# Kernel optimization log

Hardware: AMD Instinct MI355X
Metric: run time of the kernel (lower is better)

## Reference

```python
import jax, jax.numpy as jnp
import numpy as np
import itertools

# ---- constants matching init_kwargs ----
ED, KD, NH, AR = 512, 16, 8, 4
D = AR * KD            # 64 == ED // NH (required by cascade residual add)
DH = D * NH            # 512
RES, WS = 28, 7
SCALE = KD ** -0.5
KS = [7, 5, 3, 3, 3, 3, 3, 3]

# relative-position bias index map for a WSxWS window (49 unique |offset| pairs)
def _bias_idx(ws):
    pts = list(itertools.product(range(ws), range(ws)))
    offs, idxs = {}, []
    for p1 in pts:
        for p2 in pts:
            o = (abs(p1[0] - p2[0]), abs(p1[1] - p2[1]))
            if o not in offs:
                offs[o] = len(offs)
            idxs.append(offs[o])
    return np.array(idxs, dtype=np.int32).reshape(ws * ws, ws * ws), len(offs)
BIAS_IDX, N_OFFS = _bias_idx(WS)  # [49,49], 49


def dwconv(x, w, b):
    """Depthwise conv, stride 1, SAME padding (pad = k//2, odd k). w: [C,1,k,k]."""
    y = jax.lax.conv_general_dilated(x, w, (1, 1), 'SAME',
                                     dimension_numbers=('NCHW', 'OIHW', 'NCHW'),
                                     feature_group_count=x.shape[1])
    return y + b[None, :, None, None]


def pw(x, w, b):
    """1x1 conv (fused Conv2d_BN in eval mode). w: [O,C]."""
    return jnp.einsum('bchw,oc->bohw', x, w) + b[None, :, None, None]


def mlp(x, w1, b1, w2, b2):
    return pw(jax.nn.hard_swish(pw(x, w1, b1)), w2, b2)


def window_partition(x, ws):
    B, C, H, W = x.shape
    nH, nW = H // ws, W // ws
    return x.reshape(B, C, nH, ws, nW, ws).transpose(0, 2, 4, 1, 3, 5).reshape(B * nH * nW, C, ws, ws)


def window_merge(xw, B, H, W, ws):
    nH, nW = H // ws, W // ws
    C = xw.shape[1]
    return xw.reshape(B, nH, nW, C, ws, ws).transpose(0, 3, 1, 4, 2, 5).reshape(B, C, H, W)


def cascade_attention(xw, qkv_w, qkv_b, dwq_ws, dwq_bs, ab, proj_w, proj_b):
    """xw: [Bw, ED, WS, WS]; ab: [NH, N, N] bias table gathered per head."""
    Bw, C, H, W = xw.shape
    N = H * W
    spx = jnp.split(xw, NH, axis=1)          # NH chunks of [Bw, ED//NH, H, W]
    sp = spx[0]
    outs = []
    for i in range(NH):  # heads are structurally distinct (kernel sizes) -> Python loop ok
        if i > 0:
            sp = sp + spx[i]
        y = pw(sp, qkv_w[i], qkv_b[i])       # [Bw, 2*KD+D, H, W]
        q, k, v = jnp.split(y, [KD, 2 * KD], axis=1)
        q = dwconv(q, dwq_ws[i], dwq_bs[i])  # per-head depthwise conv on q
        qf = q.reshape(Bw, KD, N)
        kf = k.reshape(Bw, KD, N)
        vf = v.reshape(Bw, D, N)
        attn = jnp.einsum('bcn,bcm->bnm', qf, kf) * SCALE + ab[i]
        attn = jax.nn.softmax(attn, axis=-1)
        sp = jnp.einsum('bdm,bnm->bdn', vf, attn).reshape(Bw, D, H, W)
        outs.append(sp)
    y = jnp.concatenate(outs, axis=1)        # [Bw, DH, H, W]
    y = jax.nn.hard_swish(y)                 # proj = Sequential(act, Conv2d_BN)
    return pw(y, proj_w, proj_b)


def _forward(x, dw0_w, dw0_b, ffn0_w1, ffn0_b1, ffn0_w2, ffn0_b2,
             qkv_w, qkv_b, dwq_w7, dwq_b7, dwq_w5, dwq_b5, dwq_w3, dwq_b3,
             attn_bias, proj_w, proj_b,
             dw1_w, dw1_b, ffn1_w1, ffn1_b1, ffn1_w2, ffn1_b2):
    B, C, H, W = x.shape
    dwq_ws = [dwq_w7, dwq_w5] + [dwq_w3[i] for i in range(6)]
    dwq_bs = [dwq_b7, dwq_b5] + [dwq_b3[i] for i in range(6)]
    ab = attn_bias[:, BIAS_IDX]              # [NH, 49, 49]
    x = x + dwconv(x, dw0_w, dw0_b)
    x = x + mlp(x, ffn0_w1, ffn0_b1, ffn0_w2, ffn0_b2)
    xw = window_partition(x, WS)
    aw = cascade_attention(xw, qkv_w, qkv_b, dwq_ws, dwq_bs, ab, proj_w, proj_b)
    x = x + window_merge(aw, B, H, W, WS)
    x = x + dwconv(x, dw1_w, dw1_b)
    x = x + mlp(x, ffn1_w1, ffn1_b1, ffn1_w2, ffn1_b2)
    return x


def setup_inputs() -> dict:
    key = jax.random.key(0)
    ks = jax.random.split(key, 24)
    B = 64
    r = lambda k, shape, s=0.05: (jax.random.normal(k, shape, dtype=jnp.float32) * s)
    qkv_out = 2 * KD + D  # 96
    inp = {
        'x': jax.random.normal(ks[0], (B, ED, RES, RES), dtype=jnp.float32),
        'dw0_w': r(ks[1], (ED, 1, 3, 3)), 'dw0_b': r(ks[2], (ED,)),
        'ffn0_w1': r(ks[3], (2 * ED, ED)), 'ffn0_b1': r(ks[4], (2 * ED,)),
        'ffn0_w2': r(ks[5], (ED, 2 * ED)), 'ffn0_b2': r(ks[6], (ED,)),
        'qkv_w': r(ks[7], (NH, qkv_out, ED // NH)), 'qkv_b': r(ks[8], (NH, qkv_out)),
        'dwq_w7': r(ks[9], (KD, 1, 7, 7)), 'dwq_b7': r(ks[10], (KD,)),
        'dwq_w5': r(ks[11], (KD, 1, 5, 5)), 'dwq_b5': r(ks[12], (KD,)),
        'dwq_w3': r(ks[13], (6, KD, 1, 3, 3)), 'dwq_b3': r(ks[14], (6, KD)),
        'attn_bias': r(ks[15], (NH, N_OFFS)),
        'proj_w': r(ks[16], (ED, DH)), 'proj_b': r(ks[17], (ED,)),
        'dw1_w': r(ks[18], (ED, 1, 3, 3)), 'dw1_b': r(ks[19], (ED,)),
        'ffn1_w1': r(ks[20], (2 * ED, ED)), 'ffn1_b1': r(ks[21], (2 * ED,)),
        'ffn1_w2': r(ks[22], (ED, 2 * ED)), 'ffn1_b2': r(ks[23], (ED,)),
    }
    return inp


def reference(x, dw0_w, dw0_b, ffn0_w1, ffn0_b1, ffn0_w2, ffn0_b2,
              qkv_w, qkv_b, dwq_w7, dwq_b7, dwq_w5, dwq_b5, dwq_w3, dwq_b3,
              attn_bias, proj_w, proj_b,
              dw1_w, dw1_b, ffn1_w1, ffn1_b1, ffn1_w2, ffn1_b2):
    return _forward(x, dw0_w, dw0_b, ffn0_w1, ffn0_b1, ffn0_w2, ffn0_b2,
                    qkv_w, qkv_b, dwq_w7, dwq_b7, dwq_w5, dwq_b5, dwq_w3, dwq_b3,
                    attn_bias, proj_w, proj_b,
                    dw1_w, dw1_b, ffn1_w1, ffn1_b1, ffn1_w2, ffn1_b2)
```

## Files before the change

kernel.cpp:

```cpp
#include <hip/hip_runtime.h>
#include <hip/hip_bf16.h>


#define NPOS 50176
#define NEL ((size_t)512 * NPOS)

typedef __hip_bfloat16 hbf;
typedef __attribute__((ext_vector_type(8))) short short8;
typedef __attribute__((ext_vector_type(4))) short bf16x4;
typedef __attribute__((ext_vector_type(4))) float f32x4;

__device__ __forceinline__ float hswish(float v) {
    float t = fminf(fmaxf(v + 3.0f, 0.0f), 6.0f);
    return v * t * (1.0f / 6.0f);
}
__device__ __forceinline__ float b2f(hbf x) { return __bfloat162float(x); }
__device__ __forceinline__ hbf f2b(float x) { return __float2bfloat16(x); }

__device__ __forceinline__ unsigned short bfb(float v) {
    hbf h = f2b(v); unsigned short u; __builtin_memcpy(&u, &h, 2); return u;
}
__device__ __forceinline__ unsigned pk2(float a, float b) {
    return (unsigned)bfb(a) | ((unsigned)bfb(b) << 16);
}
__device__ __forceinline__ int swz128(int row, int b) {
    return row * 128 + (b ^ ((row & 7) << 4));
}

__device__ __forceinline__ bool is_bf16_buf(const void* probe) {
    const unsigned* w = (const unsigned*)probe;
    int hits = 0;
#pragma unroll
    for (int i = 0; i < 64; i++) {
        unsigned lo = w[i] & 0xFFFFu;
        unsigned e = (lo >> 7) & 0xFFu;
        hits += ((e >= 100u && e <= 140u) || lo == 0u) ? 1 : 0;
    }
    return hits >= 32;
}

#define OFF_W01  0
#define OFF_W02  524288
#define OFF_W11  1048576
#define OFF_W12  1572864
#define OFF_PW   2097152
#define OFF_QKVW 2359296
#define OFF_QKVB 2408448
#define OFF_W7   2409216
#define OFF_B7   2410000
#define OFF_W5   2410016
#define OFF_B5   2410416
#define OFF_W3   2410432
#define OFF_B3   2411296
#define OFF_AB   2411392
#define OFF_D0W  2411784
#define OFF_D0B  2416392
#define OFF_D1W  2416904
#define OFF_D1B  2421512
#define OFF_B01  2422024
#define OFF_B02  2423048
#define OFF_B11  2423560
#define OFF_B12  2424584
#define OFF_PB   2425096
#define ARENA_TOT 2425608

struct CvtArgs { const void* src; int off; int count; };
struct CvtTable { CvtArgs t[23]; };

__global__ __launch_bounds__(256) void k_convert(CvtTable tab, hbf* __restrict__ arena,
                                                 const void* __restrict__ probe) {
    CvtArgs a = tab.t[blockIdx.y];
    int i = blockIdx.x * 256 + threadIdx.x;
    if (i >= a.count) return;
    bool isbf = is_bf16_buf(probe);
    float v = isbf ? b2f(((const hbf*)a.src)[i]) : ((const float*)a.src)[i];
    arena[a.off + i] = f2b(v);
}

template <int EPI, int K>
__global__ __launch_bounds__(256) void k_gemm(const hbf* __restrict__ A,
                                              const hbf* __restrict__ B,
                                              const hbf* __restrict__ bias,
                                              const void* __restrict__ res,
                                              void* __restrict__ out,
                                              const void* __restrict__ probe) {
    __shared__ short sA[128 * 40];
    __shared__ short sB[128 * 40];

    const int tid = threadIdx.x;
    const int wave = tid >> 6, lane = tid & 63;
    const int col = lane & 15, quad = lane >> 4;
    const int m0 = blockIdx.x * 128, n0 = blockIdx.y * 128;
    const int wm = (wave & 1) * 64, wn = (wave >> 1) * 64;

    const int r0 = tid >> 2, c0 = tid & 3;
    const int r1 = 64 + (tid >> 2), c1 = tid & 3;

    f32x4 acc[4][4];
#pragma unroll
    for (int i = 0; i < 4; i++)
#pragma unroll
        for (int j = 0; j < 4; j++) acc[i][j] = (f32x4){0.f, 0.f, 0.f, 0.f};

    short8 pA0 = *(const short8*)(A + (size_t)(m0 + r0) * K + c0 * 8);
    short8 pA1 = *(const short8*)(A + (size_t)(m0 + r1) * K + c1 * 8);
    short8 pB0 = *(const short8*)(B + (size_t)(n0 + r0) * K + c0 * 8);
    short8 pB1 = *(const short8*)(B + (size_t)(n0 + r1) * K + c1 * 8);

    for (int k0 = 0; k0 < K; k0 += 32) {
        __syncthreads();
        *(short8*)(sA + r0 * 40 + c0 * 8) = pA0;
        *(short8*)(sA + r1 * 40 + c1 * 8) = pA1;
        *(short8*)(sB + r0 * 40 + c0 * 8) = pB0;
        *(short8*)(sB + r1 * 40 + c1 * 8) = pB1;
        if (k0 + 32 < K) {
            pA0 = *(const short8*)(A + (size_t)(m0 + r0) * K + k0 + 32 + c0 * 8);
            pA1 = *(const short8*)(A + (size_t)(m0 + r1) * K + k0 + 32 + c1 * 8);
            pB0 = *(const short8*)(B + (size_t)(n0 + r0) * K + k0 + 32 + c0 * 8);
            pB1 = *(const short8*)(B + (size_t)(n0 + r1) * K + k0 + 32 + c1 * 8);
        }
        __syncthreads();

        short8 af[4], bfr[4];
#pragma unroll
        for (int i = 0; i < 4; i++)
            af[i] = *(const short8*)(sA + (wm + i * 16 + col) * 40 + quad * 8);
#pragma unroll
        for (int j = 0; j < 4; j++)
            bfr[j] = *(const short8*)(sB + (wn + j * 16 + col) * 40 + quad * 8);
#pragma unroll
        for (int i = 0; i < 4; i++)
#pragma unroll
            for (int j = 0; j < 4; j++)
                acc[i][j] = __builtin_amdgcn_mfma_f32_16x16x32_bf16(af[i], bfr[j], acc[i][j], 0, 0, 0);
    }

    bool outbf = false;
    if constexpr (EPI == 3) outbf = is_bf16_buf(probe);

#pragma unroll
    for (int i = 0; i < 4; i++) {
#pragma unroll
        for (int j = 0; j < 4; j++) {
#pragma unroll
            for (int r = 0; r < 4; r++) {
                int mi = m0 + wm + i * 16 + quad * 4 + r;
                int nj = n0 + wn + j * 16 + col;
                float v = acc[i][j][r];
                if constexpr (EPI == 0) {
                    v = hswish(v + b2f(bias[nj]));
                    ((hbf*)out)[(size_t)mi * 1024 + nj] = f2b(v);
                } else if constexpr (EPI == 1) {
                    v += b2f(bias[mi]) + b2f(((const hbf*)res)[(size_t)nj * 512 + mi]);
                    ((float*)out)[(size_t)mi * NPOS + nj] = v;
                } else if constexpr (EPI == 2) {
                    int w = nj / 49, p = nj % 49;
                    int nct = (w >> 4) * 784 + (((w >> 2) & 3) * 7 + p / 7) * 28 + (w & 3) * 7 + p % 7;
                    size_t oi = (size_t)mi * NPOS + nct;
                    v += b2f(bias[mi]) + ((const float*)res)[oi];
                    ((float*)out)[oi] = v;
                } else {
                    int b = nj / 784, hw = nj % 784;
                    v += b2f(bias[mi]) + ((const float*)res)[(size_t)mi * NPOS + nj];
                    size_t oi = ((size_t)b * 512 + mi) * 784 + hw;
                    if (outbf) ((hbf*)out)[oi] = f2b(v);
                    else ((float*)out)[oi] = v;
                }
            }
        }
    }
}

template <int MODE, bool ISBF>
__device__ void dw_body(float* sIn, float* sW, const void* __restrict__ in,
                        const hbf* __restrict__ w, const hbf* __restrict__ bias,
                        hbf* __restrict__ outNK, float* __restrict__ outCT) {
    const int tid = threadIdx.x;
    const int tx = tid & 63, tg = tid >> 6;
    const int n0 = blockIdx.x * 64, c0 = blockIdx.y * 64;

    for (int e = tid; e < 640; e += 256) {
        int cc = e / 10, t = e - cc * 10;
        sW[e] = (t < 9) ? b2f(w[(c0 + cc) * 9 + t]) : b2f(bias[c0 + cc]);
    }

#pragma unroll
    for (int k = 0; k < 8; k++) {
        int idx = tid + k * 256;
        int ch = idx >> 5, j4 = idx & 31;
        int p = n0 - 32 + j4 * 4;
        p = p < 0 ? 0 : (p > NPOS - 4 ? NPOS - 4 : p);
        f32x4 v;
        if constexpr (MODE == 1) {
            v = *(const f32x4*)((const float*)in + (size_t)(c0 + ch) * NPOS + p);
        } else {
            int b = p / 784, hw = p - b * 784;
            size_t ix = ((size_t)b * 512 + c0 + ch) * 784 + hw;
            if constexpr (ISBF) {
                bf16x4 t4 = *(const bf16x4*)((const hbf*)in + ix);
#pragma unroll
                for (int j = 0; j < 4; j++) {
                    unsigned u = (unsigned)(unsigned short)t4[j] << 16;
                    v[j] = __uint_as_float(u);
                }
            } else {
                v = *(const f32x4*)((const float*)in + ix);
            }
        }
        *(f32x4*)(sIn + ch * 128 + j4 * 4) = v;
    }
    __syncthreads();

    const int n = n0 + tx;
    const int b = n / 784, hw = n - b * 784;
    const int r = hw / 28, s = hw - r * 28;
    const float mrow[3] = { r > 0 ? 1.f : 0.f, 1.f, r < 27 ? 1.f : 0.f };
    const float mcol[3] = { s > 0 ? 1.f : 0.f, 1.f, s < 27 ? 1.f : 0.f };

    float vals[16];
#pragma unroll
    for (int i = 0; i < 16; i++) {
        const int cc = tg + 4 * i;
        const float* row = sIn + cc * 128 + 32 + tx;
        float acc = sW[cc * 10 + 9];
        float center = row[0];
#pragma unroll
        for (int dy = 0; dy < 3; dy++)
#pragma unroll
            for (int dx = 0; dx < 3; dx++)
                acc = fmaf(row[(dy - 1) * 28 + (dx - 1)],
                           mrow[dy] * mcol[dx] * sW[cc * 10 + dy * 3 + dx], acc);
        float val = center + acc;
        vals[i] = val;
        if constexpr (MODE == 1) outCT[(size_t)(c0 + cc) * NPOS + n] = val;
    }
    __syncthreads();

    float (*tile)[65] = (float (*)[65])sIn;
#pragma unroll
    for (int i = 0; i < 16; i++) tile[tg + 4 * i][tx] = vals[i];
    __syncthreads();
    for (int q = tg; q < 64; q += 4)
        outNK[(size_t)(n0 + q) * 512 + c0 + tx] = f2b(tile[tx][q]);
}

template <int MODE>
__global__ __launch_bounds__(256, 4) void k_dw(const void* in, const hbf* w, const hbf* b,
                                               hbf* outNK, float* outCT, const void* probe) {
    __shared__ float sIn[64 * 128];
    __shared__ float sW[64 * 10];
    if constexpr (MODE == 1) {
        dw_body<1, false>(sIn, sW, in, w, b, outNK, outCT);
    } else {
        if (is_bf16_buf(probe)) dw_body<0, true>(sIn, sW, in, w, b, outNK, outCT);
        else dw_body<0, false>(sIn, sW, in, w, b, outNK, outCT);
    }
}

__global__ __launch_bounds__(256, 4) void k_attn(const float* __restrict__ y2,
                                                 const hbf* __restrict__ arena,
                                                 hbf* __restrict__ ywin) {
    __shared__ short spT[64 * 64];
    __shared__ short vbT[64 * 64];
    __shared__ short atb[64 * 64];
    __shared__ short qT[64 * 40];
    __shared__ short kT[64 * 40];
    __shared__ float qraw[16 * 52];
    __shared__ float abf[8 * 49];

    const int tid = threadIdx.x;
    const int wave = tid >> 6, lane = tid & 63;
    const int col = lane & 15, quad = lane >> 4;
    const int w = blockIdx.x;
    const int wb = w >> 4, wh = (w >> 2) & 3, ww = w & 3;
    const size_t base = (size_t)wb * 784 + (wh * 7) * 28 + ww * 7;

    for (int e = tid; e < 64 * 64; e += 256) { vbT[e] = 0; atb[e] = 0; }
    for (int e = tid; e < 64 * 16; e += 256) {
        int n = e >> 4, c = 16 + (e & 15);
        qT[n * 40 + c] = 0; kT[n * 40 + c] = 0;
    }
    for (int e = tid; e < 8 * 49; e += 256) abf[e] = b2f(arena[OFF_AB + e]);

    for (int e = tid; e < 64 * 49; e += 256) {
        int c = e / 49, n = e - c * 49;
        float v = y2[(size_t)c * NPOS + base + (n / 7) * 28 + (n % 7)];
        *(hbf*)((char*)spT + swz128(n, 2 * c)) = f2b(v);
    }

    int nj[4], posj[4], m7[4], mm7[4];
    bool vj[4];
#pragma unroll
    for (int j = 0; j < 4; j++) {
        nj[j] = j * 16 + col;
        vj[j] = nj[j] < 49;
        int nc = vj[j] ? nj[j] : 48;
        m7[j] = nc / 7; mm7[j] = nc - m7[j] * 7;
        posj[j] = m7[j] * 28 + mm7[j];
    }
    const int nq = wave * 16 + quad * 4;

#pragma unroll 1
    for (int h = 0; h < 8; h++) {
        __syncthreads();

        const hbf* wq = arena + OFF_QKVW + h * 96 * 64;
        const int brow = wave * 16 + col;
        short8 sb0 = *(const short8*)((const char*)spT + swz128(brow, quad * 16));
        short8 sb1 = *(const short8*)((const char*)spT + swz128(brow, 64 + quad * 16));
        f32x4 yacc[6];
#pragma unroll
        for (int i = 0; i < 6; i++) {
            short8 a0 = *(const short8*)(wq + (i * 16 + col) * 64 + quad * 8);
            short8 a1 = *(const short8*)(wq + (i * 16 + col) * 64 + 32 + quad * 8);
            f32x4 z = (f32x4){0.f, 0.f, 0.f, 0.f};
            z = __builtin_amdgcn_mfma_f32_16x16x32_bf16(a0, sb0, z, 0, 0, 0);
            z = __builtin_amdgcn_mfma_f32_16x16x32_bf16(a1, sb1, z, 0, 0, 0);
            yacc[i] = z;
        }
        if (brow < 49) {
            const int n = brow;
#pragma unroll
            for (int i = 0; i < 6; i++) {
                float vv[4];
#pragma unroll
                for (int r = 0; r < 4; r++)
                    vv[r] = yacc[i][r] + b2f(arena[OFF_QKVB + h * 96 + i * 16 + quad * 4 + r]);
                if (i == 0) {
#pragma unroll
                    for (int r = 0; r < 4; r++) qraw[(quad * 4 + r) * 52 + n] = vv[r];
                } else if (i == 1) {
                    *(unsigned*)((char*)kT + n * 80 + 8 * quad)     = pk2(vv[0], vv[1]);
                    *(unsigned*)((char*)kT + n * 80 + 8 * quad + 4) = pk2(vv[2], vv[3]);
                } else {
#pragma unroll
                    for (int r = 0; r < 4; r++) {
                        int d = (i - 2) * 16 + quad * 4 + r;
                        *(hbf*)((char*)vbT + swz128(d, 2 * n)) = f2b(vv[r]);
                    }
                }
            }
        }
        __syncthreads();

        const hbf* cw; const hbf* cb; int ks;
        if (h == 0)      { cw = arena + OFF_W7; cb = arena + OFF_B7; ks = 7; }
        else if (h == 1) { cw = arena + OFF_W5; cb = arena + OFF_B5; ks = 5; }
        else             { cw = arena + OFF_W3 + (h - 2) * 144; cb = arena + OFF_B3 + (h - 2) * 16; ks = 3; }
        const int pad = ks >> 1;
        for (int e = tid; e < 784; e += 256) {
            int c = e / 49, n = e - c * 49;
            int r = n / 7, s = n - r * 7;
            float acc = b2f(cb[c]);
            for (int dy = 0; dy < ks; dy++) {
                int rr = r + dy - pad;
                if (rr < 0 || rr >= 7) continue;
                for (int dx = 0; dx < ks; dx++) {
                    int ss = s + dx - pad;
                    if (ss < 0 || ss >= 7) continue;
                    acc += b2f(cw[c * ks * ks + dy * ks + dx]) * qraw[c * 52 + rr * 7 + ss];
                }
            }
            *(hbf*)((char*)qT + n * 80 + 2 * c) = f2b(acc * 0.25f);
        }
        __syncthreads();

        short8 qa = *(const short8*)((const char*)qT + (wave * 16 + col) * 80 + quad * 16);
        f32x4 sat[4];
#pragma unroll
        for (int j = 0; j < 4; j++) {
            short8 kb = *(const short8*)((const char*)kT + (j * 16 + col) * 80 + quad * 16);
            f32x4 z = (f32x4){0.f, 0.f, 0.f, 0.f};
            sat[j] = __builtin_amdgcn_mfma_f32_16x16x32_bf16(qa, kb, z, 0, 0, 0);
        }
#pragma unroll
        for (int r = 0; r < 4; r++) {
            int n = nq + r;
            int ncl = n < 49 ? n : 48;
            int n7 = ncl / 7, nn7 = ncl - n7 * 7;
            float v0 = sat[0][r] + abf[h * 49 + abs(n7 - m7[0]) * 7 + abs(nn7 - mm7[0])];
            float v1 = sat[1][r] + abf[h * 49 + abs(n7 - m7[1]) * 7 + abs(nn7 - mm7[1])];
            float v2 = sat[2][r] + abf[h * 49 + abs(n7 - m7[2]) * 7 + abs(nn7 - mm7[2])];
            float v3 = (col == 0) ? sat[3][r] + abf[h * 49 + abs(n7 - m7[3]) * 7 + abs(nn7 - mm7[3])]
                                  : -1e30f;
            float mx = fmaxf(fmaxf(v0, v1), fmaxf(v2, v3));
#pragma unroll
            for (int s = 1; s < 16; s <<= 1) mx = fmaxf(mx, __shfl_xor(mx, s));
            float p0 = __expf(v0 - mx), p1 = __expf(v1 - mx), p2 = __expf(v2 - mx);
            float p3 = (col == 0) ? __expf(v3 - mx) : 0.f;
            float sm = p0 + p1 + p2 + p3;
#pragma unroll
            for (int s = 1; s < 16; s <<= 1) sm += __shfl_xor(sm, s);
            float inv = 1.0f / sm;
            *(hbf*)((char*)atb + swz128(n, 2 * col))        = f2b(p0 * inv);
            *(hbf*)((char*)atb + swz128(n, 2 * (16 + col))) = f2b(p1 * inv);
            *(hbf*)((char*)atb + swz128(n, 2 * (32 + col))) = f2b(p2 * inv);
            if (col == 0) *(hbf*)((char*)atb + swz128(n, 2 * 48)) = f2b(p3 * inv);
        }
        __syncthreads();

        short8 va0 = *(const short8*)((const char*)vbT + swz128(wave * 16 + col, quad * 16));
        short8 va1 = *(const short8*)((const char*)vbT + swz128(wave * 16 + col, 64 + quad * 16));
#pragma unroll
        for (int j = 0; j < 4; j++) {
            short8 pb0 = *(const short8*)((const char*)atb + swz128(nj[j], quad * 16));
            short8 pb1 = *(const short8*)((const char*)atb + swz128(nj[j], 64 + quad * 16));
            f32x4 o = (f32x4){0.f, 0.f, 0.f, 0.f};
            o = __builtin_amdgcn_mfma_f32_16x16x32_bf16(va0, pb0, o, 0, 0, 0);
            o = __builtin_amdgcn_mfma_f32_16x16x32_bf16(va1, pb1, o, 0, 0, 0);
            if (vj[j]) {
                size_t yo = ((size_t)w * 49 + nj[j]) * 512 + h * 64 + nq;
                *(unsigned*)(ywin + yo)     = pk2(hswish(o[0]), hswish(o[1]));
                *(unsigned*)(ywin + yo + 2) = pk2(hswish(o[2]), hswish(o[3]));
                if (h < 7) {
                    const float* ys = y2 + (size_t)((h + 1) * 64 + nq) * NPOS + base + posj[j];
                    unsigned s0 = pk2(o[0] + ys[0],
                                      o[1] + ys[(size_t)NPOS]);
                    unsigned s1 = pk2(o[2] + ys[2 * (size_t)NPOS],
                                      o[3] + ys[3 * (size_t)NPOS]);
                    *(unsigned*)((char*)spT + swz128(nj[j], 2 * nq))     = s0;
                    *(unsigned*)((char*)spT + swz128(nj[j], 2 * nq + 4)) = s1;
                }
            }
        }
    }
}


extern "C" void kernel_launch(void* const* d_in, const int* in_sizes, int n_in,
                              void* d_out, int out_size, void* d_ws, size_t ws_size,
                              hipStream_t stream) {
    const void* x = d_in[0];

    if (ws_size < NEL * 10 + (size_t)ARENA_TOT * 2) return;

    uint8_t* p = (uint8_t*)d_ws;
    hbf*   R0 = (hbf*)p;
    hbf*   R1 = (hbf*)(p + NEL * 2);
    float* R2 = (float*)(p + NEL * 6);
    hbf*   arena = (hbf*)(p + NEL * 10);

    hbf*   y1t  = R0;
    hbf*   hid  = R1;
    float* y2f  = R2;
    hbf*   ywin = R0;
    float* x3f  = (float*)R1;
    float* x4f  = R2;
    hbf*   x4t  = R0;
    hbf*   hid2 = R1;

    CvtTable tab = {{
        { d_in[3],  OFF_W01,  524288 },
        { d_in[5],  OFF_W02,  524288 },
        { d_in[20], OFF_W11,  524288 },
        { d_in[22], OFF_W12,  524288 },
        { d_in[16], OFF_PW,   262144 },
        { d_in[7],  OFF_QKVW, 49152 },
        { d_in[8],  OFF_QKVB, 768 },
        { d_in[9],  OFF_W7,   784 },
        { d_in[10], OFF_B7,   16 },
        { d_in[11], OFF_W5,   400 },
        { d_in[12], OFF_B5,   16 },
        { d_in[13], OFF_W3,   864 },
        { d_in[14], OFF_B3,   96 },
        { d_in[15], OFF_AB,   392 },
        { d_in[1],  OFF_D0W,  4608 },
        { d_in[2],  OFF_D0B,  512 },
        { d_in[18], OFF_D1W,  4608 },
        { d_in[19], OFF_D1B,  512 },
        { d_in[4],  OFF_B01,  1024 },
        { d_in[6],  OFF_B02,  512 },
        { d_in[21], OFF_B11,  1024 },
        { d_in[23], OFF_B12,  512 },
        { d_in[17], OFF_PB,   512 },
    }};

    dim3 blk(256);

    k_convert<<<dim3(2048, 23), blk, 0, stream>>>(tab, arena, x);
    k_dw<0><<<dim3(NPOS / 64, 8), blk, 0, stream>>>(x, arena + OFF_D0W, arena + OFF_D0B, y1t, nullptr, x);
    k_gemm<0, 512><<<dim3(392, 8), blk, 0, stream>>>(y1t, arena + OFF_W01, arena + OFF_B01, nullptr, hid, x);
    k_gemm<1, 1024><<<dim3(4, 392), blk, 0, stream>>>(arena + OFF_W02, hid, arena + OFF_B02, y1t, y2f, x);
    k_attn<<<1024, blk, 0, stream>>>(y2f, arena, ywin);
    k_gemm<2, 512><<<dim3(4, 392), blk, 0, stream>>>(arena + OFF_PW, ywin, arena + OFF_PB, y2f, x3f, x);
    k_dw<1><<<dim3(NPOS / 64, 8), blk, 0, stream>>>(x3f, arena + OFF_D1W, arena + OFF_D1B, x4t, x4f, x);
    k_gemm<0, 512><<<dim3(392, 8), blk, 0, stream>>>(x4t, arena + OFF_W11, arena + OFF_B11, nullptr, hid2, x);
    k_gemm<3, 1024><<<dim3(4, 392), blk, 0, stream>>>(arena + OFF_W12, hid2, arena + OFF_B12, x4f, d_out, x);
}
```

Measured before the change: 1.143 ms.

## Load GEMM tiles directly to LDS with swizzle and prefetch cascade residuals

The GEMM main loop now uses global_load_lds to copy A/B tiles straight into shared memory, with an XOR-swizzled 64-wide K layout and K-step 64 (two MFMA sub-steps per barrier). This replaces the register-staged software prefetch, removing VGPR staging and halving the number of barriers. In exchange the global loads are no longer overlapped with compute across iterations. Separately, the attention kernel now issues the next head's residual loads from y2 at the top of each head iteration, so their latency overlaps the QKV and softmax work.

```diff
diff --git a/kernel.cpp b/kernel.cpp
--- a/kernel.cpp
+++ b/kernel.cpp
@@ -6,6 +6,7 @@
 #define NEL ((size_t)512 * NPOS)
 
 typedef __hip_bfloat16 hbf;
+typedef unsigned int u32;
 typedef __attribute__((ext_vector_type(8))) short short8;
 typedef __attribute__((ext_vector_type(4))) short bf16x4;
 typedef __attribute__((ext_vector_type(4))) float f32x4;
@@ -25,6 +26,11 @@
 }
 __device__ __forceinline__ int swz128(int row, int b) {
     return row * 128 + (b ^ ((row & 7) << 4));
+}
+__device__ __forceinline__ void gl16(const hbf* g, short* l) {
+    __builtin_amdgcn_global_load_lds((const __attribute__((address_space(1))) u32*)g,
+                                     (__attribute__((address_space(3))) u32*)l,
+                                     16, 0, 0);
 }
 
 __device__ __forceinline__ bool is_bf16_buf(const void* probe) {
@@ -84,8 +90,8 @@
                                               const void* __restrict__ res,
                                               void* __restrict__ out,
                                               const void* __restrict__ probe) {
-    __shared__ short sA[128 * 40];
-    __shared__ short sB[128 * 40];
+    __shared__ short sA[128 * 64];
+    __shared__ short sB[128 * 64];
 
     const int tid = threadIdx.x;
     const int wave = tid >> 6, lane = tid & 63;
@@ -93,8 +99,12 @@
     const int m0 = blockIdx.x * 128, n0 = blockIdx.y * 128;
     const int wm = (wave & 1) * 64, wn = (wave >> 1) * 64;
 
-    const int r0 = tid >> 2, c0 = tid & 3;
-    const int r1 = 64 + (tid >> 2), c1 = tid & 3;
+    const int rowl = lane >> 3;
+    const int kswz = ((lane & 7) ^ rowl) * 8;
+    const hbf* Ag = A + (size_t)(m0 + wave * 32 + rowl) * K + kswz;
+    const hbf* Bg = B + (size_t)(n0 + wave * 32 + rowl) * K + kswz;
+    short* sAw = sA + (wave * 32) * 64;
+    short* sBw = sB + (wave * 32) * 64;
 
     f32x4 acc[4][4];
 #pragma unroll
@@ -102,37 +112,34 @@
 #pragma unroll
         for (int j = 0; j < 4; j++) acc[i][j] = (f32x4){0.f, 0.f, 0.f, 0.f};
 
-    short8 pA0 = *(const short8*)(A + (size_t)(m0 + r0) * K + c0 * 8);
-    short8 pA1 = *(const short8*)(A + (size_t)(m0 + r1) * K + c1 * 8);
-    short8 pB0 = *(const short8*)(B + (size_t)(n0 + r0) * K + c0 * 8);
-    short8 pB1 = *(const short8*)(B + (size_t)(n0 + r1) * K + c1 * 8);
-
-    for (int k0 = 0; k0 < K; k0 += 32) {
+    for (int k0 = 0; k0 < K; k0 += 64) {
         __syncthreads();
-        *(short8*)(sA + r0 * 40 + c0 * 8) = pA0;
-        *(short8*)(sA + r1 * 40 + c1 * 8) = pA1;
-        *(short8*)(sB + r0 * 40 + c0 * 8) = pB0;
-        *(short8*)(sB + r1 * 40 + c1 * 8) = pB1;
-        if (k0 + 32 < K) {
-            pA0 = *(const short8*)(A + (size_t)(m0 + r0) * K + k0 + 32 + c0 * 8);
-            pA1 = *(const short8*)(A + (size_t)(m0 + r1) * K + k0 + 32 + c1 * 8);
-            pB0 = *(const short8*)(B + (size_t)(n0 + r0) * K + k0 + 32 + c0 * 8);
-            pB1 = *(const short8*)(B + (size_t)(n0 + r1) * K + k0 + 32 + c1 * 8);
+#pragma unroll
+        for (int t = 0; t < 4; t++) {
+            gl16(Ag + k0 + (size_t)t * 8 * K, sAw + t * 8 * 64);
+            gl16(Bg + k0 + (size_t)t * 8 * K, sBw + t * 8 * 64);
         }
         __syncthreads();
 
-        short8 af[4], bfr[4];
-#pragma unroll
-        for (int i = 0; i < 4; i++)
-            af[i] = *(const short8*)(sA + (wm + i * 16 + col) * 40 + quad * 8);
-#pragma unroll
-        for (int j = 0; j < 4; j++)
-            bfr[j] = *(const short8*)(sB + (wn + j * 16 + col) * 40 + quad * 8);
-#pragma unroll
-        for (int i = 0; i < 4; i++)
-#pragma unroll
-            for (int j = 0; j < 4; j++)
-                acc[i][j] = __builtin_amdgcn_mfma_f32_16x16x32_bf16(af[i], bfr[j], acc[i][j], 0, 0, 0);
+#pragma unroll
+        for (int kk = 0; kk < 2; kk++) {
+            short8 af[4], bfr[4];
+#pragma unroll
+            for (int i = 0; i < 4; i++) {
+                int r = wm + i * 16 + col;
+                af[i] = *(const short8*)(sA + r * 64 + (((kk * 4 + quad) ^ (r & 7)) * 8));
+            }
+#pragma unroll
+            for (int j = 0; j < 4; j++) {
+                int r = wn + j * 16 + col;
+                bfr[j] = *(const short8*)(sB + r * 64 + (((kk * 4 + quad) ^ (r & 7)) * 8));
+            }
+#pragma unroll
+            for (int i = 0; i < 4; i++)
+#pragma unroll
+                for (int j = 0; j < 4; j++)
+                    acc[i][j] = __builtin_amdgcn_mfma_f32_16x16x32_bf16(af[i], bfr[j], acc[i][j], 0, 0, 0);
+        }
     }
 
     bool outbf = false;
@@ -302,6 +309,17 @@
 
 #pragma unroll 1
     for (int h = 0; h < 8; h++) {
+        float pre[4][4];
+        if (h < 7) {
+#pragma unroll
+            for (int j = 0; j < 4; j++) {
+                if (vj[j]) {
+                    const float* ys = y2 + (size_t)((h + 1) * 64 + nq) * NPOS + base + posj[j];
+#pragma unroll
+                    for (int r = 0; r < 4; r++) pre[j][r] = ys[r * (size_t)NPOS];
+                }
+            }
+        }
         __syncthreads();
 
         const hbf* wq = arena + OFF_QKVW + h * 96 * 64;
@@ -413,11 +431,8 @@
                 *(unsigned*)(ywin + yo)     = pk2(hswish(o[0]), hswish(o[1]));
                 *(unsigned*)(ywin + yo + 2) = pk2(hswish(o[2]), hswish(o[3]));
                 if (h < 7) {
-                    const float* ys = y2 + (size_t)((h + 1) * 64 + nq) * NPOS + base + posj[j];
-                    unsigned s0 = pk2(o[0] + ys[0],
-                                      o[1] + ys[(size_t)NPOS]);
-                    unsigned s1 = pk2(o[2] + ys[2 * (size_t)NPOS],
-                                      o[3] + ys[3 * (size_t)NPOS]);
+                    unsigned s0 = pk2(o[0] + pre[j][0], o[1] + pre[j][1]);
+                    unsigned s1 = pk2(o[2] + pre[j][2], o[3] + pre[j][3]);
                     *(unsigned*)((char*)spT + swz128(nj[j], 2 * nq))     = s0;
                     *(unsigned*)((char*)spT + swz128(nj[j], 2 * nq + 4)) = s1;
                 }
```

Result: no change. 1.139 ms (-0.3%).
